# Performance work log

Measured on AMD Instinct MI355X. Metric: run time of the kernel, lower is better.

## Reference

```python
import jax, jax.numpy as jnp
import numpy as np

B, S, E, H = 2, 2048, 1024, 16
D = E // H
SCALE = D ** -0.5


def setup_inputs() -> dict:
    key = jax.random.key(0)
    k1, k2, k3, k4, k5 = jax.random.split(key, 5)
    x = jax.random.normal(k1, (B, S, E), dtype=jnp.float32)
    # torch Linear weights: [out, in]
    W_attn = jax.random.normal(k2, (3 * E, E), dtype=jnp.float32) * (E ** -0.5)
    b_attn = jax.random.normal(k3, (3 * E,), dtype=jnp.float32) * 0.02
    W_proj = jax.random.normal(k4, (E, E), dtype=jnp.float32) * (E ** -0.5)
    b_proj = jax.random.normal(k5, (E,), dtype=jnp.float32) * 0.02
    mask = jnp.tril(jnp.ones((S, S), dtype=jnp.int32))[None, None]  # causal [1,1,S,S]
    return {"x": x, "W_attn": W_attn, "b_attn": b_attn,
            "W_proj": W_proj, "b_proj": b_proj, "mask": mask}


def reference(x, W_attn, b_attn, W_proj, b_proj, mask):
    # fused qkv projection: [B,S,3E]
    qkv = jnp.einsum('bse,fe->bsf', x, W_attn) + b_attn
    q, k, v = jnp.split(qkv, 3, axis=-1)
    # split heads -> [B,H,S,D]
    def heads(t):
        return t.reshape(B, S, H, D).transpose(0, 2, 1, 3)
    q, k, v = heads(q), heads(k), heads(v)
    # scaled dot-product attention with causal mask
    w = jnp.einsum('bhqd,bhkd->bhqk', q, k) * SCALE
    w = jnp.where(mask == 0, jnp.finfo(w.dtype).min, w)
    w = jax.nn.softmax(w, axis=-1)  # attn dropout p=0 (eval)
    o = jnp.einsum('bhqk,bhkd->bhqd', w, v)
    # merge heads -> [B,S,E]
    o = o.transpose(0, 2, 1, 3).reshape(B, S, E)
    out = jnp.einsum('bse,fe->bsf', o, W_proj) + b_proj  # resid dropout p=0
    return out
```

## Files before the change

### kernel.cpp

```cpp
#include <hip/hip_runtime.h>
#include <hip/hip_bf16.h>

typedef unsigned short u16;
typedef unsigned int u32;
typedef float f32x4 __attribute__((ext_vector_type(4)));
typedef short bf16x8 __attribute__((ext_vector_type(8)));

#define BB 2
#define SS 2048
#define EE 1024
#define HH 16
#define DD 64
#define QSCALE 0.18033688011f

__device__ __forceinline__ u16 f2bf(float f) {
    union { u32 i; float f; } x; x.f = f;
    return (u16)((x.i + 0x7FFFu + ((x.i >> 16) & 1u)) >> 16);
}
__device__ __forceinline__ u32 pkbf(float a, float b) {
    __hip_bfloat162 h = __float22bfloat162_rn(make_float2(a, b));
    union { __hip_bfloat162 h; u32 u; } c; c.h = h; return c.u;
}

#define MFMA16(a, b, c) __builtin_amdgcn_mfma_f32_16x16x32_bf16((a), (b), (c), 0, 0, 0)

__device__ __forceinline__ void gld16(const u16* g, u16* l) {
    __builtin_amdgcn_global_load_lds(
        (const __attribute__((address_space(1))) void*)g,
        (__attribute__((address_space(3))) void*)l,
        16, 0, 0);
}

__global__ __launch_bounds__(256) void convert_all(
    const float* __restrict__ x, const float* __restrict__ wa,
    const float* __restrict__ wp, u16* __restrict__ dst)
{
    const size_t n0 = (size_t)4096 * 1024;
    const size_t n1 = n0 + (size_t)3072 * 1024;
    size_t i = ((size_t)blockIdx.x * 256 + threadIdx.x) * 4;
    const float* s;
    size_t off;
    if (i < n0)      { s = x;  off = 0;  }
    else if (i < n1) { s = wa; off = n0; }
    else             { s = wp; off = n1; }
    float4 v = *(const float4*)(s + (i - off));
    uint2 o;
    o.x = pkbf(v.x, v.y);
    o.y = pkbf(v.z, v.w);
    *(uint2*)(dst + i) = o;
}

__global__ __launch_bounds__(512, 6) void gemm_qkv(
    const u16* __restrict__ A, const u16* __restrict__ B, const float* __restrict__ bias,
    u16* __restrict__ Qo, u16* __restrict__ Ko, u16* __restrict__ Vto)
{
    __shared__ __align__(16) u16 SMEM[16384];
    u16* As = SMEM;
    u16* Bs = SMEM + 8192;
    const int n0 = blockIdx.x * 128, m0 = blockIdx.y * 128;
    const int tid = threadIdx.x;
    const int wave = tid >> 6, lane = tid & 63;
    const int l16 = lane & 15, quad = lane >> 4;
    const int wm = wave >> 2, wn = wave & 3;
    const int ldr = lane >> 3;
    const int csw = ((lane & 7) ^ ldr) * 8;

    f32x4 acc[4][2];
#pragma unroll
    for (int i = 0; i < 4; ++i)
#pragma unroll
        for (int j = 0; j < 2; ++j) acc[i][j] = f32x4{0.f, 0.f, 0.f, 0.f};

    const int aorb = wave >> 2;
    u16* stgbuf = aorb ? Bs : As;
    const u16* stgsrc = aorb ? B : A;
    const int stgbase = aorb ? n0 : m0;

    for (int k0 = 0; k0 < 1024; k0 += 64) {
        __syncthreads();
#pragma unroll
        for (int t = 0; t < 4; ++t) {
            const int c = (wave & 3) * 4 + t;
            const int row = c * 8 + ldr;
            gld16(stgsrc + (size_t)(stgbase + row) * 1024 + k0 + csw,
                  &stgbuf[c * 512 + lane * 8]);
        }
        __syncthreads();
#pragma unroll
        for (int ks = 0; ks < 2; ++ks) {
            bf16x8 af[4], bf[2];
#pragma unroll
            for (int i = 0; i < 4; ++i)
                af[i] = *(const bf16x8*)&As[(wm * 64 + i * 16 + l16) * 64 +
                                            ((ks * 4 + quad) ^ (l16 & 7)) * 8];
#pragma unroll
            for (int j = 0; j < 2; ++j)
                bf[j] = *(const bf16x8*)&Bs[(wn * 32 + j * 16 + l16) * 64 +
                                            ((ks * 4 + quad) ^ (l16 & 7)) * 8];
#pragma unroll
            for (int i = 0; i < 4; ++i)
#pragma unroll
                for (int j = 0; j < 2; ++j)
                    acc[i][j] = MFMA16(af[i], bf[j], acc[i][j]);
        }
    }

    const int part = blockIdx.x >> 3;
    const int hbase = (blockIdx.x & 7) << 1;
    if (part != 2) {
        const int h = hbase + (wn >> 1);
#pragma unroll
        for (int j = 0; j < 2; ++j) {
            const int f = n0 + wn * 32 + j * 16 + l16;
            const int d = f & 63;
            const float bj = bias[f];
#pragma unroll
            for (int i = 0; i < 4; ++i) {
#pragma unroll
                for (int r = 0; r < 4; ++r) {
                    const int m = m0 + wm * 64 + i * 16 + quad * 4 + r;
                    const int b = m >> 11, s = m & 2047;
                    const float val = acc[i][j][r] + bj;
                    if (part == 0)
                        Qo[(((size_t)(b * HH + h)) * SS + s) * DD + d] = f2bf(val * QSCALE);
                    else
                        Ko[(((size_t)(b * HH + h)) * SS + s) * DD + d] = f2bf(val);
                }
            }
        }
    } else {
        u16* T = SMEM;
#pragma unroll
        for (int wmr = 0; wmr < 2; ++wmr) {
            __syncthreads();
            if (wm == wmr) {
#pragma unroll
                for (int j = 0; j < 2; ++j) {
                    const float bj = bias[n0 + wn * 32 + j * 16 + l16];
#pragma unroll
                    for (int i = 0; i < 4; ++i) {
                        uint2 pw;
                        pw.x = pkbf(acc[i][j][0] + bj, acc[i][j][1] + bj);
                        pw.y = pkbf(acc[i][j][2] + bj, acc[i][j][3] + bj);
                        *(uint2*)&T[(wn * 32 + j * 16 + l16) * 72 + i * 16 + quad * 4] = pw;
                    }
                }
            }
            __syncthreads();
            const int frow = tid >> 2;
            const int qtr = tid & 3;
            const int h = hbase + (frow >> 6);
            const int d = frow & 63;
            const int mg = m0 + wmr * 64;
            const int b = mg >> 11, sbase = mg & 2047;
            u16* dstrow = Vto + (((size_t)(b * HH + h)) * DD + d) * SS + sbase;
#pragma unroll
            for (int l = 0; l < 4; ++l) {
                const int mo = qtr * 16 + l * 4;
                *(uint2*)(dstrow + mo) = *(const uint2*)&T[frow * 72 + mo];
            }
        }
    }
}

__global__ __launch_bounds__(512, 4) void gemm_proj(
    const u16* __restrict__ A, const u16* __restrict__ B, const float* __restrict__ bias,
    float* __restrict__ out)
{
    __shared__ __align__(16) u16 SMEM[2][12288];
    const int n0 = blockIdx.y * 128, m0 = blockIdx.x * 64;
    const int tid = threadIdx.x;
    const int wave = tid >> 6, lane = tid & 63;
    const int l16 = lane & 15, quad = lane >> 4;
    const int wm = wave >> 2, wn = wave & 3;
    const int ldr = lane >> 3;
    const int csw = ((lane & 7) ^ ldr) * 8;

    f32x4 acc[2][2];
#pragma unroll
    for (int i = 0; i < 2; ++i)
#pragma unroll
        for (int j = 0; j < 2; ++j) acc[i][j] = f32x4{0.f, 0.f, 0.f, 0.f};

    auto stage = [&](int k0, int buf) {
#pragma unroll
        for (int t = 0; t < 3; ++t) {
            const int c = wave * 3 + t;
            if (c < 8) {
                const int row = c * 8 + ldr;
                gld16(A + (size_t)(m0 + row) * 1024 + k0 + csw,
                      &SMEM[buf][c * 512 + lane * 8]);
            } else {
                const int c2 = c - 8;
                const int row = c2 * 8 + ldr;
                gld16(B + (size_t)(n0 + row) * 1024 + k0 + csw,
                      &SMEM[buf][4096 + c2 * 512 + lane * 8]);
            }
        }
    };

    stage(0, 0);
    for (int k0 = 0; k0 < 1024; k0 += 64) {
        const int cur = (k0 >> 6) & 1;
        __syncthreads();
        if (k0 + 64 < 1024) stage(k0 + 64, cur ^ 1);
        const u16* As = SMEM[cur];
        const u16* Bs = SMEM[cur] + 4096;
#pragma unroll
        for (int ks = 0; ks < 2; ++ks) {
            bf16x8 af[2], bf[2];
#pragma unroll
            for (int i = 0; i < 2; ++i)
                af[i] = *(const bf16x8*)&As[(wm * 32 + i * 16 + l16) * 64 +
                                            ((ks * 4 + quad) ^ (l16 & 7)) * 8];
#pragma unroll
            for (int j = 0; j < 2; ++j)
                bf[j] = *(const bf16x8*)&Bs[(wn * 32 + j * 16 + l16) * 64 +
                                            ((ks * 4 + quad) ^ (l16 & 7)) * 8];
#pragma unroll
            for (int i = 0; i < 2; ++i)
#pragma unroll
                for (int j = 0; j < 2; ++j)
                    acc[i][j] = MFMA16(af[i], bf[j], acc[i][j]);
        }
    }
#pragma unroll
    for (int j = 0; j < 2; ++j) {
        const int f = n0 + wn * 32 + j * 16 + l16;
        const float bj = bias[f];
#pragma unroll
        for (int i = 0; i < 2; ++i) {
#pragma unroll
            for (int r = 0; r < 4; ++r) {
                const int m = m0 + wm * 32 + i * 16 + quad * 4 + r;
                out[(size_t)m * EE + f] = acc[i][j][r] + bj;
            }
        }
    }
}

__global__ __launch_bounds__(256, 2) void attn(
    const u16* __restrict__ Q, const u16* __restrict__ K, const u16* __restrict__ VT,
    u16* __restrict__ O)
{
    const int p = blockIdx.y;
    const int bh = blockIdx.x;
    const int tid = threadIdx.x;
    const int wave = tid >> 6, lane = tid & 63;
    const int l16 = lane & 15, quad = lane >> 4;
    const int ldr = lane >> 3;
    const int csw = ((lane & 7) ^ ldr) * 8;
    __shared__ __align__(16) u16 Ks[2][2][64 * 64];
    __shared__ __align__(16) u16 Vts[2][2][64 * 64];
    __shared__ __align__(16) u16 Ps[64 * 72];

    const u16* qptr = Q + (size_t)bh * SS * DD;
    const u16* kptr = K + (size_t)bh * SS * DD;
    const u16* vtptr = VT + (size_t)bh * DD * SS;
    const int b = bh >> 4, h = bh & 15;

    auto stage = [&](int t, int buf, int sub) {
#pragma unroll
        for (int c = 0; c < 2; ++c) {
            const int a0 = wave * 2 + c;
            const int row = a0 * 8 + ldr;
            gld16(kptr + (size_t)(t * 64 + row) * DD + csw,
                  &Ks[buf][sub][a0 * 512 + lane * 8]);
            gld16(vtptr + (size_t)row * SS + t * 64 + csw,
                  &Vts[buf][sub][a0 * 512 + lane * 8]);
        }
    };

    for (int half = 0; half < 2; ++half) {
        const int qb = half ? p : 31 - p;
        const int qrow = qb * 64 + wave * 16 + l16;
        bf16x8 bq[2];
#pragma unroll
        for (int ks = 0; ks < 2; ++ks)
            bq[ks] = *(const bf16x8*)(qptr + (size_t)qrow * DD + ks * 32 + quad * 8);

        float lp = 0.f;
        f32x4 o_acc[4];
#pragma unroll
        for (int j = 0; j < 4; ++j) o_acc[j] = f32x4{0.f, 0.f, 0.f, 0.f};

        auto tile_compute = [&](const u16* Kb, const u16* Vb, int t) {
            f32x4 s[4];
#pragma unroll
            for (int j = 0; j < 4; ++j) s[j] = f32x4{0.f, 0.f, 0.f, 0.f};
            __builtin_amdgcn_s_setprio(1);
#pragma unroll
            for (int ks = 0; ks < 2; ++ks) {
#pragma unroll
                for (int j = 0; j < 4; ++j) {
                    bf16x8 ak = *(const bf16x8*)&Kb[(j * 16 + l16) * 64 +
                                                    ((ks * 4 + quad) ^ (l16 & 7)) * 8];
                    s[j] = MFMA16(ak, bq[ks], s[j]);
                }
            }
            __builtin_amdgcn_s_setprio(0);
            if (t == qb) {
#pragma unroll
                for (int j = 0; j < 4; ++j)
#pragma unroll
                    for (int r = 0; r < 4; ++r) {
                        const int key = t * 64 + j * 16 + quad * 4 + r;
                        if (key > qrow) s[j][r] = -INFINITY;
                    }
            }
#pragma unroll
            for (int j = 0; j < 4; ++j) {
                const float p0 = __builtin_amdgcn_exp2f(s[j][0]);
                const float p1 = __builtin_amdgcn_exp2f(s[j][1]);
                const float p2 = __builtin_amdgcn_exp2f(s[j][2]);
                const float p3 = __builtin_amdgcn_exp2f(s[j][3]);
                lp += (p0 + p1) + (p2 + p3);
                uint2 pw; pw.x = pkbf(p0, p1); pw.y = pkbf(p2, p3);
                *(uint2*)&Ps[(wave * 16 + l16) * 72 + j * 16 + quad * 4] = pw;
            }
            __builtin_amdgcn_s_setprio(1);
#pragma unroll
            for (int ks = 0; ks < 2; ++ks) {
                bf16x8 bp = *(const bf16x8*)&Ps[(wave * 16 + l16) * 72 + ks * 32 + quad * 8];
#pragma unroll
                for (int j = 0; j < 4; ++j) {
                    bf16x8 av = *(const bf16x8*)&Vb[(j * 16 + l16) * 64 +
                                                    ((ks * 4 + quad) ^ (l16 & 7)) * 8];
                    o_acc[j] = MFMA16(av, bp, o_acc[j]);
                }
            }
            __builtin_amdgcn_s_setprio(0);
        };

        __syncthreads();
        stage(0, 0, 0);
        stage(qb < 1 ? qb : 1, 0, 1);

        for (int kb = 0; kb <= qb; kb += 2) {
            const int cur = (kb >> 1) & 1;
            __syncthreads();
            if (kb + 2 <= qb) {
                stage(kb + 2, cur ^ 1, 0);
                const int t3 = kb + 3 > qb ? qb : kb + 3;
                stage(t3, cur ^ 1, 1);
            }
            tile_compute(Ks[cur][0], Vts[cur][0], kb);
            if (kb + 1 <= qb)
                tile_compute(Ks[cur][1], Vts[cur][1], kb + 1);
        }

        float l = lp;
        l += __shfl_xor(l, 16);
        l += __shfl_xor(l, 32);
        const float inv = 1.0f / l;
#pragma unroll
        for (int j = 0; j < 4; ++j) {
            uint2 o4;
            o4.x = pkbf(o_acc[j][0] * inv, o_acc[j][1] * inv);
            o4.y = pkbf(o_acc[j][2] * inv, o_acc[j][3] * inv);
            *(uint2*)&O[((size_t)(b * SS + qrow)) * EE + h * DD + j * 16 + quad * 4] = o4;
        }
    }
}

extern "C" void kernel_launch(void* const* d_in, const int* in_sizes, int n_in,
                              void* d_out, int out_size, void* d_ws, size_t ws_size,
                              hipStream_t stream) {
    const float* x      = (const float*)d_in[0];
    const float* W_attn = (const float*)d_in[1];
    const float* b_attn = (const float*)d_in[2];
    const float* W_proj = (const float*)d_in[3];
    const float* b_proj = (const float*)d_in[4];
    float* out = (float*)d_out;

    u16* xb  = (u16*)d_ws;
    u16* wab = xb + (size_t)4096 * 1024;
    u16* wpb = wab + (size_t)3072 * 1024;
    u16* qw  = wpb + (size_t)1024 * 1024;
    u16* kw  = qw + (size_t)BB * HH * SS * DD;
    u16* vtw = kw + (size_t)BB * HH * SS * DD;
    u16* ow  = xb;

    convert_all<<<8192, 256, 0, stream>>>(x, W_attn, W_proj, xb);
    gemm_qkv<<<dim3(24, 32), 512, 0, stream>>>(xb, wab, b_attn, qw, kw, vtw);
    attn<<<dim3(32, 16), 256, 0, stream>>>(qw, kw, vtw, ow);
    gemm_proj<<<dim3(64, 8), 512, 0, stream>>>(ow, wpb, b_proj, out);
}
```

Before: 174.4 us.

## Fuse fp32-to-bf16 conversion into GEMM staging loads, drop convert kernel

```diff
diff --git a/kernel.cpp b/kernel.cpp
--- a/kernel.cpp
+++ b/kernel.cpp
@@ -31,27 +31,8 @@
         16, 0, 0);
 }
 
-__global__ __launch_bounds__(256) void convert_all(
-    const float* __restrict__ x, const float* __restrict__ wa,
-    const float* __restrict__ wp, u16* __restrict__ dst)
-{
-    const size_t n0 = (size_t)4096 * 1024;
-    const size_t n1 = n0 + (size_t)3072 * 1024;
-    size_t i = ((size_t)blockIdx.x * 256 + threadIdx.x) * 4;
-    const float* s;
-    size_t off;
-    if (i < n0)      { s = x;  off = 0;  }
-    else if (i < n1) { s = wa; off = n0; }
-    else             { s = wp; off = n1; }
-    float4 v = *(const float4*)(s + (i - off));
-    uint2 o;
-    o.x = pkbf(v.x, v.y);
-    o.y = pkbf(v.z, v.w);
-    *(uint2*)(dst + i) = o;
-}
-
-__global__ __launch_bounds__(512, 6) void gemm_qkv(
-    const u16* __restrict__ A, const u16* __restrict__ B, const float* __restrict__ bias,
+__global__ __launch_bounds__(512, 4) void gemm_qkv(
+    const float* __restrict__ A, const float* __restrict__ B, const float* __restrict__ bias,
     u16* __restrict__ Qo, u16* __restrict__ Ko, u16* __restrict__ Vto)
 {
     __shared__ __align__(16) u16 SMEM[16384];
@@ -72,9 +53,9 @@
         for (int j = 0; j < 2; ++j) acc[i][j] = f32x4{0.f, 0.f, 0.f, 0.f};
 
     const int aorb = wave >> 2;
+    const float* stgsrc = aorb ? B : A;
+    const int stgbase = aorb ? n0 : m0;
     u16* stgbuf = aorb ? Bs : As;
-    const u16* stgsrc = aorb ? B : A;
-    const int stgbase = aorb ? n0 : m0;
 
     for (int k0 = 0; k0 < 1024; k0 += 64) {
         __syncthreads();
@@ -82,8 +63,13 @@
         for (int t = 0; t < 4; ++t) {
             const int c = (wave & 3) * 4 + t;
             const int row = c * 8 + ldr;
-            gld16(stgsrc + (size_t)(stgbase + row) * 1024 + k0 + csw,
-                  &stgbuf[c * 512 + lane * 8]);
+            const float* sp = stgsrc + (size_t)(stgbase + row) * 1024 + k0 + csw;
+            float4 va = *(const float4*)sp;
+            float4 vb = *(const float4*)(sp + 4);
+            uint4 w;
+            w.x = pkbf(va.x, va.y); w.y = pkbf(va.z, va.w);
+            w.z = pkbf(vb.x, vb.y); w.w = pkbf(vb.z, vb.w);
+            *(uint4*)&stgbuf[c * 512 + lane * 8] = w;
         }
         __syncthreads();
 #pragma unroll
@@ -164,7 +150,7 @@
 }
 
 __global__ __launch_bounds__(512, 4) void gemm_proj(
-    const u16* __restrict__ A, const u16* __restrict__ B, const float* __restrict__ bias,
+    const u16* __restrict__ A, const float* __restrict__ B, const float* __restrict__ bias,
     float* __restrict__ out)
 {
     __shared__ __align__(16) u16 SMEM[2][12288];
@@ -193,8 +179,13 @@
             } else {
                 const int c2 = c - 8;
                 const int row = c2 * 8 + ldr;
-                gld16(B + (size_t)(n0 + row) * 1024 + k0 + csw,
-                      &SMEM[buf][4096 + c2 * 512 + lane * 8]);
+                const float* sp = B + (size_t)(n0 + row) * 1024 + k0 + csw;
+                float4 va = *(const float4*)sp;
+                float4 vb = *(const float4*)(sp + 4);
+                uint4 w;
+                w.x = pkbf(va.x, va.y); w.y = pkbf(va.z, va.w);
+                w.z = pkbf(vb.x, vb.y); w.w = pkbf(vb.z, vb.w);
+                *(uint4*)&SMEM[buf][4096 + c2 * 512 + lane * 8] = w;
             }
         }
     };
@@ -373,16 +364,12 @@
     const float* b_proj = (const float*)d_in[4];
     float* out = (float*)d_out;
 
-    u16* xb  = (u16*)d_ws;
-    u16* wab = xb + (size_t)4096 * 1024;
-    u16* wpb = wab + (size_t)3072 * 1024;
-    u16* qw  = wpb + (size_t)1024 * 1024;
+    u16* ow  = (u16*)d_ws;
+    u16* qw  = ow + (size_t)BB * SS * EE;
     u16* kw  = qw + (size_t)BB * HH * SS * DD;
     u16* vtw = kw + (size_t)BB * HH * SS * DD;
-    u16* ow  = xb;
-
-    convert_all<<<8192, 256, 0, stream>>>(x, W_attn, W_proj, xb);
-    gemm_qkv<<<dim3(24, 32), 512, 0, stream>>>(xb, wab, b_attn, qw, kw, vtw);
+
+    gemm_qkv<<<dim3(24, 32), 512, 0, stream>>>(x, W_attn, b_attn, qw, kw, vtw);
     attn<<<dim3(32, 16), 256, 0, stream>>>(qw, kw, vtw, ow);
-    gemm_proj<<<dim3(64, 8), 512, 0, stream>>>(ow, wpb, b_proj, out);
-}
+    gemm_proj<<<dim3(64, 8), 512, 0, stream>>>(ow, W_proj, b_proj, out);
+}
```

Result: slower. 206.8 us (+18.6%).

## Split attention keys across waves and keep P in registers with cross-wave reduction

Applied to the files above, without the earlier changes.

```diff
diff --git a/kernel.cpp b/kernel.cpp
--- a/kernel.cpp
+++ b/kernel.cpp
@@ -250,9 +250,10 @@
     const int l16 = lane & 15, quad = lane >> 4;
     const int ldr = lane >> 3;
     const int csw = ((lane & 7) ^ ldr) * 8;
-    __shared__ __align__(16) u16 Ks[2][2][64 * 64];
-    __shared__ __align__(16) u16 Vts[2][2][64 * 64];
-    __shared__ __align__(16) u16 Ps[64 * 72];
+    __shared__ __align__(16) u16 SMEM[32768];
+    __shared__ float Lred[4][64];
+    u16* const Ksb = SMEM;
+    u16* const Vtb = SMEM + 16384;
 
     const u16* qptr = Q + (size_t)bh * SS * DD;
     const u16* kptr = K + (size_t)bh * SS * DD;
@@ -265,72 +266,29 @@
             const int a0 = wave * 2 + c;
             const int row = a0 * 8 + ldr;
             gld16(kptr + (size_t)(t * 64 + row) * DD + csw,
-                  &Ks[buf][sub][a0 * 512 + lane * 8]);
+                  Ksb + (buf * 2 + sub) * 4096 + a0 * 512 + lane * 8);
             gld16(vtptr + (size_t)row * SS + t * 64 + csw,
-                  &Vts[buf][sub][a0 * 512 + lane * 8]);
+                  Vtb + (buf * 2 + sub) * 4096 + a0 * 512 + lane * 8);
         }
     };
 
     for (int half = 0; half < 2; ++half) {
         const int qb = half ? p : 31 - p;
-        const int qrow = qb * 64 + wave * 16 + l16;
-        bf16x8 bq[2];
-#pragma unroll
-        for (int ks = 0; ks < 2; ++ks)
-            bq[ks] = *(const bf16x8*)(qptr + (size_t)qrow * DD + ks * 32 + quad * 8);
-
-        float lp = 0.f;
-        f32x4 o_acc[4];
-#pragma unroll
-        for (int j = 0; j < 4; ++j) o_acc[j] = f32x4{0.f, 0.f, 0.f, 0.f};
-
-        auto tile_compute = [&](const u16* Kb, const u16* Vb, int t) {
-            f32x4 s[4];
-#pragma unroll
-            for (int j = 0; j < 4; ++j) s[j] = f32x4{0.f, 0.f, 0.f, 0.f};
-            __builtin_amdgcn_s_setprio(1);
-#pragma unroll
-            for (int ks = 0; ks < 2; ++ks) {
-#pragma unroll
-                for (int j = 0; j < 4; ++j) {
-                    bf16x8 ak = *(const bf16x8*)&Kb[(j * 16 + l16) * 64 +
-                                                    ((ks * 4 + quad) ^ (l16 & 7)) * 8];
-                    s[j] = MFMA16(ak, bq[ks], s[j]);
-                }
-            }
-            __builtin_amdgcn_s_setprio(0);
-            if (t == qb) {
-#pragma unroll
-                for (int j = 0; j < 4; ++j)
-#pragma unroll
-                    for (int r = 0; r < 4; ++r) {
-                        const int key = t * 64 + j * 16 + quad * 4 + r;
-                        if (key > qrow) s[j][r] = -INFINITY;
-                    }
-            }
-#pragma unroll
-            for (int j = 0; j < 4; ++j) {
-                const float p0 = __builtin_amdgcn_exp2f(s[j][0]);
-                const float p1 = __builtin_amdgcn_exp2f(s[j][1]);
-                const float p2 = __builtin_amdgcn_exp2f(s[j][2]);
-                const float p3 = __builtin_amdgcn_exp2f(s[j][3]);
-                lp += (p0 + p1) + (p2 + p3);
-                uint2 pw; pw.x = pkbf(p0, p1); pw.y = pkbf(p2, p3);
-                *(uint2*)&Ps[(wave * 16 + l16) * 72 + j * 16 + quad * 4] = pw;
-            }
-            __builtin_amdgcn_s_setprio(1);
-#pragma unroll
-            for (int ks = 0; ks < 2; ++ks) {
-                bf16x8 bp = *(const bf16x8*)&Ps[(wave * 16 + l16) * 72 + ks * 32 + quad * 8];
-#pragma unroll
-                for (int j = 0; j < 4; ++j) {
-                    bf16x8 av = *(const bf16x8*)&Vb[(j * 16 + l16) * 64 +
-                                                    ((ks * 4 + quad) ^ (l16 & 7)) * 8];
-                    o_acc[j] = MFMA16(av, bp, o_acc[j]);
-                }
-            }
-            __builtin_amdgcn_s_setprio(0);
-        };
+
+        bf16x8 bq[4][2];
+#pragma unroll
+        for (int n = 0; n < 4; ++n)
+#pragma unroll
+            for (int ks = 0; ks < 2; ++ks)
+                bq[n][ks] = *(const bf16x8*)(qptr +
+                    (size_t)(qb * 64 + n * 16 + l16) * DD + ks * 32 + quad * 8);
+
+        float lp[4] = {0.f, 0.f, 0.f, 0.f};
+        f32x4 o_acc[4][4];
+#pragma unroll
+        for (int d = 0; d < 4; ++d)
+#pragma unroll
+            for (int n = 0; n < 4; ++n) o_acc[d][n] = f32x4{0.f, 0.f, 0.f, 0.f};
 
         __syncthreads();
         stage(0, 0, 0);
@@ -341,24 +299,115 @@
             __syncthreads();
             if (kb + 2 <= qb) {
                 stage(kb + 2, cur ^ 1, 0);
-                const int t3 = kb + 3 > qb ? qb : kb + 3;
-                stage(t3, cur ^ 1, 1);
-            }
-            tile_compute(Ks[cur][0], Vts[cur][0], kb);
-            if (kb + 1 <= qb)
-                tile_compute(Ks[cur][1], Vts[cur][1], kb + 1);
-        }
-
-        float l = lp;
-        l += __shfl_xor(l, 16);
-        l += __shfl_xor(l, 32);
-        const float inv = 1.0f / l;
-#pragma unroll
-        for (int j = 0; j < 4; ++j) {
-            uint2 o4;
-            o4.x = pkbf(o_acc[j][0] * inv, o_acc[j][1] * inv);
-            o4.y = pkbf(o_acc[j][2] * inv, o_acc[j][3] * inv);
-            *(uint2*)&O[((size_t)(b * SS + qrow)) * EE + h * DD + j * 16 + quad * 4] = o4;
+                stage(kb + 3 > qb ? qb : kb + 3, cur ^ 1, 1);
+            }
+
+            u32 pk[2][4][2];
+#pragma unroll
+            for (int sub = 0; sub < 2; ++sub) {
+                const int t = kb + sub;
+                f32x4 s[4];
+                if (t <= qb) {
+#pragma unroll
+                    for (int n = 0; n < 4; ++n) s[n] = f32x4{0.f, 0.f, 0.f, 0.f};
+                    const u16* Kc = Ksb + (cur * 2 + sub) * 4096;
+                    __builtin_amdgcn_s_setprio(1);
+#pragma unroll
+                    for (int ks = 0; ks < 2; ++ks) {
+                        bf16x8 ak = *(const bf16x8*)&Kc[(wave * 16 + l16) * 64 +
+                                        ((ks * 4 + quad) ^ (l16 & 7)) * 8];
+#pragma unroll
+                        for (int n = 0; n < 4; ++n)
+                            s[n] = MFMA16(ak, bq[n][ks], s[n]);
+                    }
+                    __builtin_amdgcn_s_setprio(0);
+                    if (t == qb) {
+#pragma unroll
+                        for (int n = 0; n < 4; ++n)
+#pragma unroll
+                            for (int r = 0; r < 4; ++r) {
+                                const int key = t * 64 + wave * 16 + quad * 4 + r;
+                                const int qq  = qb * 64 + n * 16 + l16;
+                                if (key > qq) s[n][r] = -INFINITY;
+                            }
+                    }
+                } else {
+#pragma unroll
+                    for (int n = 0; n < 4; ++n)
+                        s[n] = f32x4{-INFINITY, -INFINITY, -INFINITY, -INFINITY};
+                }
+#pragma unroll
+                for (int n = 0; n < 4; ++n) {
+                    const float p0 = __builtin_amdgcn_exp2f(s[n][0]);
+                    const float p1 = __builtin_amdgcn_exp2f(s[n][1]);
+                    const float p2 = __builtin_amdgcn_exp2f(s[n][2]);
+                    const float p3 = __builtin_amdgcn_exp2f(s[n][3]);
+                    lp[n] += (p0 + p1) + (p2 + p3);
+                    pk[sub][n][0] = pkbf(p0, p1);
+                    pk[sub][n][1] = pkbf(p2, p3);
+                }
+            }
+
+            bf16x8 bp[4];
+#pragma unroll
+            for (int n = 0; n < 4; ++n) {
+                union { u32 w[4]; bf16x8 v; } u;
+                u.w[0] = pk[0][n][0]; u.w[1] = pk[0][n][1];
+                u.w[2] = pk[1][n][0]; u.w[3] = pk[1][n][1];
+                bp[n] = u.v;
+            }
+            const int vsw = ((wave * 2 + (quad >> 1)) ^ (l16 & 7)) * 8 + (quad & 1) * 4;
+            __builtin_amdgcn_s_setprio(1);
+#pragma unroll
+            for (int d = 0; d < 4; ++d) {
+                union { uint2 u2[2]; bf16x8 v; } a;
+                a.u2[0] = *(const uint2*)&Vtb[(cur * 2 + 0) * 4096 + (d * 16 + l16) * 64 + vsw];
+                a.u2[1] = *(const uint2*)&Vtb[(cur * 2 + 1) * 4096 + (d * 16 + l16) * 64 + vsw];
+#pragma unroll
+                for (int n = 0; n < 4; ++n)
+                    o_acc[d][n] = MFMA16(a.v, bp[n], o_acc[d][n]);
+            }
+            __builtin_amdgcn_s_setprio(0);
+        }
+
+#pragma unroll
+        for (int n = 0; n < 4; ++n) {
+            lp[n] += __shfl_xor(lp[n], 16);
+            lp[n] += __shfl_xor(lp[n], 32);
+        }
+        __syncthreads();
+        if (quad == 0) {
+#pragma unroll
+            for (int n = 0; n < 4; ++n) Lred[wave][n * 16 + l16] = lp[n];
+        }
+        float* Ored = (float*)SMEM;
+#pragma unroll
+        for (int d = 0; d < 4; ++d)
+#pragma unroll
+            for (int n = 0; n < 4; ++n) {
+                const int chunk = (d * 4 + quad) ^ (l16 & 7);
+                *(f32x4*)&Ored[wave * 4096 + (n * 16 + l16) * 64 + chunk * 4] = o_acc[d][n];
+            }
+        __syncthreads();
+        {
+            const int q = wave * 16 + (lane >> 2);
+            const int dg = lane & 3;
+            const float l = Lred[0][q] + Lred[1][q] + Lred[2][q] + Lred[3][q];
+            const float inv = 1.0f / l;
+            u32 wout[8];
+#pragma unroll
+            for (int dv = 0; dv < 4; ++dv) {
+                const int chunk = (dg * 4 + dv) ^ (q & 7);
+                f32x4 acc = f32x4{0.f, 0.f, 0.f, 0.f};
+#pragma unroll
+                for (int w = 0; w < 4; ++w)
+                    acc += *(const f32x4*)&Ored[w * 4096 + q * 64 + chunk * 4];
+                wout[dv * 2 + 0] = pkbf(acc[0] * inv, acc[1] * inv);
+                wout[dv * 2 + 1] = pkbf(acc[2] * inv, acc[3] * inv);
+            }
+            u16* dst = O + ((size_t)(b * SS + qb * 64 + q)) * EE + h * DD + dg * 16;
+            *(uint4*)dst = *(const uint4*)&wout[0];
+            *(uint4*)(dst + 8) = *(const uint4*)&wout[4];
         }
     }
 }
```

Measured after the change: 172.2 us. About the same (-1.3%).
